# Optimization experiments

Measured on AMD Instinct MI355X. Metric: run time of the kernel, lower is better.

The kernel has to match this reference:

```python
import jax, jax.numpy as jnp
import numpy as np
from jax import lax

AB = np.array([[-37.254833,-82.50967,53.254833,98.50967],[-82.50967,-173.01933,98.50967,189.01933],[-173.01933,-354.03867,189.01933,370.03867],[-56.,-56.,72.,72.],[-120.,-120.,136.,136.],[-248.,-248.,264.,264.],[-82.50967,-37.254833,98.50967,53.254833],[-173.01933,-82.50967,189.01933,98.50967],[-354.03867,-173.01933,370.03867,189.01933]],dtype=np.float32)
STRIDE = 16
PRE = 2000    # pre-NMS proposals
POST = 300    # post-NMS proposals
NMS_T = 0.7

def conv(x, w, stride, pad):
    return lax.conv_general_dilated(x, w, (stride, stride), pad,
                                    dimension_numbers=('NCHW', 'OIHW', 'NCHW'))

def setup_inputs() -> dict:
    k = jax.random.split(jax.random.key(0), 16)
    f32 = jnp.float32
    def W(i, shape, fan):
        return jax.random.normal(k[i], shape, f32) / np.sqrt(fan)
    return {
        'x':    jax.random.normal(k[0], (1, 3, 608, 1008), f32),
        'Wext': W(1, (512, 3, 16, 16), 3 * 16 * 16),        # stand-in stride-16 extractor
        'Wc1':  W(2, (512, 512, 3, 3), 512 * 9), 'bc1': jnp.zeros((512,), f32),
        'Wloc': W(3, (36, 512, 1, 1), 512) * 0.1, 'bloc': jnp.zeros((36,), f32),
        'Wsc':  W(4, (18, 512, 1, 1), 512), 'bsc': jnp.zeros((18,), f32),
        'W1':   W(5, (25088, 4096), 25088), 'b1': jnp.zeros((4096,), f32),
        'W2':   W(6, (4096, 4096), 4096),  'b2': jnp.zeros((4096,), f32),
        'Wl':   W(7, (4096, 84), 4096),    'bl': jnp.zeros((84,), f32),
        'Ws':   W(8, (4096, 21), 4096),    'bs': jnp.zeros((21,), f32),
        'scale': 2,
    }

def _anchors(h, w):
    yy = jnp.arange(h, dtype=jnp.float32) * STRIDE
    xx = jnp.arange(w, dtype=jnp.float32) * STRIDE
    sy, sx = jnp.meshgrid(yy, xx, indexing='ij')
    shift = jnp.stack([sy.ravel(), sx.ravel(), sy.ravel(), sx.ravel()], axis=1)  # [h*w,4]
    return (jnp.asarray(AB)[None, :, :] + shift[:, None, :]).reshape(-1, 4)      # [h*w*9,4]

def _loc2bbox(a, loc):
    ph = a[:, 2] - a[:, 0]; pw = a[:, 3] - a[:, 1]
    py = a[:, 0] + 0.5 * ph; px = a[:, 1] + 0.5 * pw
    cy = loc[:, 0] * ph + py; cx = loc[:, 1] * pw + px
    hh = jnp.exp(loc[:, 2]) * ph; ww = jnp.exp(loc[:, 3]) * pw
    return jnp.stack([cy - 0.5 * hh, cx - 0.5 * ww, cy + 0.5 * hh, cx + 0.5 * ww], axis=1)

def _nms(boxes, valid):
    # greedy sequential NMS, boxes pre-sorted by score desc; +1 area convention as in source
    n = boxes.shape[0]
    areas = (boxes[:, 2] - boxes[:, 0] + 1.) * (boxes[:, 3] - boxes[:, 1] + 1.)
    idx = jnp.arange(n)
    def body(i, keep):
        b = boxes[i]
        iy1 = jnp.maximum(b[0], boxes[:, 0]); ix1 = jnp.maximum(b[1], boxes[:, 1])
        iy2 = jnp.minimum(b[2], boxes[:, 2]); ix2 = jnp.minimum(b[3], boxes[:, 3])
        inter = jnp.clip(iy2 - iy1 + 1., 0) * jnp.clip(ix2 - ix1 + 1., 0)
        iou = inter / (areas[i] + areas - inter)
        sup = (iou > NMS_T) & (idx > i)
        return jnp.where(keep[i], keep & ~sup, keep)  # suppressed boxes don't suppress
    return lax.fori_loop(0, n, body, valid)

def _roi_maxpool(feat, rois):
    # feat [C,h,w]; adaptive max pool each integer ROI crop to 7x7 (matches AdaptiveMaxPool2d bins)
    C, h, w = feat.shape
    yy = jnp.arange(h); xx = jnp.arange(w); i7 = jnp.arange(7)
    NEG = jnp.float32(-1e30)
    def one(box):
        t = jnp.floor(box / STRIDE).astype(jnp.int32)
        y0 = jnp.clip(t[0], 0, h - 1); x0 = jnp.clip(t[1], 0, w - 1)
        y1 = jnp.clip(t[2], 0, h - 1); x1 = jnp.clip(t[3], 0, w - 1)
        H = y1 - y0 + 1; W_ = x1 - x0 + 1
        rs = y0 + (i7 * H) // 7;  re = y0 + ((i7 + 1) * H + 6) // 7
        cs = x0 + (i7 * W_) // 7; ce = x0 + ((i7 + 1) * W_ + 6) // 7
        rowm = (yy[None, :] >= rs[:, None]) & (yy[None, :] < re[:, None])  # [7,h]
        colm = (xx[None, :] >= cs[:, None]) & (xx[None, :] < ce[:, None])  # [7,w]
        tmp = jnp.max(jnp.where(colm[None, None, :, :], feat[:, :, None, :], NEG), axis=-1)  # [C,h,7]
        return jnp.max(jnp.where(rowm[None, :, :, None], tmp[:, None, :, :], NEG), axis=2)   # [C,7,7]
    return lax.map(one, rois)

def reference(x, Wext, Wc1, bc1, Wloc, bloc, Wsc, bsc, W1, b1, W2, b2, Wl, bl, Ws, bs, scale):
    Himg, Wimg = x.shape[2], x.shape[3]
    feat = jax.nn.relu(conv(x, Wext, STRIDE, 'VALID'))                 # [1,512,h,w]
    h, w = feat.shape[2], feat.shape[3]
    layer1 = jax.nn.relu(conv(feat, Wc1, 1, 'SAME') + bc1[None, :, None, None])
    rpn_locs = (conv(layer1, Wloc, 1, 'SAME') + bloc[None, :, None, None]).transpose(0, 2, 3, 1).reshape(-1, 4)
    sc = (conv(layer1, Wsc, 1, 'SAME') + bsc[None, :, None, None]).transpose(0, 2, 3, 1).reshape(h, w, 9, 2)
    fg = sc[..., 1].reshape(-1)
    anchor = _anchors(h, w)
    roi = _loc2bbox(anchor, rpn_locs)
    roi = jnp.stack([jnp.clip(roi[:, 0], 0, Himg), jnp.clip(roi[:, 1], 0, Wimg),
                     jnp.clip(roi[:, 2], 0, Himg), jnp.clip(roi[:, 3], 0, Wimg)], axis=1)
    min_size = 16. * scale
    valid = ((roi[:, 2] - roi[:, 0]) >= min_size) & ((roi[:, 3] - roi[:, 1]) >= min_size)
    s = jnp.where(valid, fg, -jnp.inf)      # masked instead of filtered (jit-friendly)
    order = jnp.argsort(-s)[:PRE]
    boxes = roi[order]; vb = valid[order]
    keep = _nms(boxes, vb)
    sel = jnp.argsort(jnp.where(keep, 0, PRE) + jnp.arange(PRE))[:POST]  # kept boxes first, index order
    rois = lax.stop_gradient(boxes[sel])                                 # [300,4], detached as in source
    pool = _roi_maxpool(feat[0], rois).reshape(POST, -1)                 # [300,25088]
    fc7 = jax.nn.relu(jax.nn.relu(pool @ W1 + b1) @ W2 + b2)
    return (fc7 @ Wl + bl, fc7 @ Ws + bs, rois)
```

## Files before the change

### kernel.cpp

```cpp
#include <hip/hip_runtime.h>
#include <stdint.h>

#define FH 38
#define FW 63
#define NPOS 2394
#define NANCH 21546
#define HIMG 608
#define WIMG 1008
#define PRE 2000
#define POST 300

typedef __attribute__((ext_vector_type(8))) short bf16x8;
typedef __attribute__((ext_vector_type(4))) float f32x4;

__device__ __constant__ float c_AB[9][4] = {
  {-37.254833f,-82.50967f,53.254833f,98.50967f},
  {-82.50967f,-173.01933f,98.50967f,189.01933f},
  {-173.01933f,-354.03867f,189.01933f,370.03867f},
  {-56.f,-56.f,72.f,72.f},
  {-120.f,-120.f,136.f,136.f},
  {-248.f,-248.f,264.f,264.f},
  {-82.50967f,-37.254833f,98.50967f,53.254833f},
  {-173.01933f,-82.50967f,189.01933f,98.50967f},
  {-354.03867f,-173.01933f,370.03867f,189.01933f}};

__device__ __forceinline__ unsigned short f2bf(float f) {
  unsigned u = __float_as_uint(f);
  u += 0x7FFFu + ((u >> 16) & 1u);
  return (unsigned short)(u >> 16);
}

__global__ __launch_bounds__(256) void k_wc1pack(const float* __restrict__ Wc1, float* __restrict__ Bp) {
  __shared__ float t[4608];
  int o = blockIdx.x;
  const float* src = Wc1 + (size_t)o * 4608;
  for (int i = threadIdx.x; i < 4608; i += 256) t[i] = src[i];
  __syncthreads();
  float* dst = Bp + (size_t)o * 4608;
  for (int i = threadIdx.x; i < 4608; i += 256) {
    int r = i >> 9, ci = i & 511;
    dst[i] = t[ci * 9 + r];
  }
}

template<int MODE>
__global__ __launch_bounds__(256) void k_gemm_conv(
    const float* __restrict__ src, const float* __restrict__ B,
    float* __restrict__ P, int Kc)
{
  const int K = MODE ? 4608 : 768;
  __shared__ float As[16][132];
  __shared__ float Bs[16][68];
  int tid = threadIdx.x;
  int bm = blockIdx.x * 128, bn = blockIdx.y * 64;
  int k0 = blockIdx.z * Kc;
  int kend = k0 + Kc;
  int tx = tid & 15, ty = tid >> 4;
  float4 acc[8];
  #pragma unroll
  for (int i = 0; i < 8; ++i) acc[i] = make_float4(0.f, 0.f, 0.f, 0.f);
  int lr = tid >> 2, lk = (tid & 3) * 4;
  int ar0 = bm + lr;      if (ar0 >= NPOS) ar0 = NPOS - 1;
  int ar1 = bm + lr + 64; if (ar1 >= NPOS) ar1 = NPOS - 1;
  int py0 = ar0 / FW, px0 = ar0 - py0 * FW;
  int py1 = ar1 / FW, px1 = ar1 - py1 * FW;
  const float* bp = B + (size_t)(bn + lr) * K + lk;

  float4 ra0, ra1, rb;
  auto loadA = [&](int kk, float4& v0, float4& v1) {
    if (MODE == 0) {
      int ci = kk >> 8, ky = (kk >> 4) & 15;
      const float* base = src + (size_t)(ci * HIMG + ky) * WIMG + lk;
      v0 = *(const float4*)(base + (size_t)(py0 * 16) * WIMG + px0 * 16);
      v1 = *(const float4*)(base + (size_t)(py1 * 16) * WIMG + px1 * 16);
    } else {
      int r = kk >> 9, cb = (kk & 511) + lk;
      int q = r / 3;
      int dy = q - 1, dx = r - q * 3 - 1;
      int yy0 = py0 + dy, xx0 = px0 + dx;
      int yy1 = py1 + dy, xx1 = px1 + dx;
      v0 = ((unsigned)yy0 < FH && (unsigned)xx0 < FW)
           ? *(const float4*)(src + (((size_t)(yy0 * FW + xx0)) << 9) + cb)
           : make_float4(0.f, 0.f, 0.f, 0.f);
      v1 = ((unsigned)yy1 < FH && (unsigned)xx1 < FW)
           ? *(const float4*)(src + (((size_t)(yy1 * FW + xx1)) << 9) + cb)
           : make_float4(0.f, 0.f, 0.f, 0.f);
    }
  };
  loadA(k0, ra0, ra1);
  rb = *(const float4*)(bp + k0);

  for (; k0 < kend; k0 += 16) {
    As[lk + 0][lr] = ra0.x; As[lk + 1][lr] = ra0.y; As[lk + 2][lr] = ra0.z; As[lk + 3][lr] = ra0.w;
    As[lk + 0][lr + 64] = ra1.x; As[lk + 1][lr + 64] = ra1.y; As[lk + 2][lr + 64] = ra1.z; As[lk + 3][lr + 64] = ra1.w;
    Bs[lk + 0][lr] = rb.x; Bs[lk + 1][lr] = rb.y; Bs[lk + 2][lr] = rb.z; Bs[lk + 3][lr] = rb.w;
    __syncthreads();
    if (k0 + 16 < kend) {
      loadA(k0 + 16, ra0, ra1);
      rb = *(const float4*)(bp + k0 + 16);
    }
    #pragma unroll
    for (int k = 0; k < 16; ++k) {
      float4 aL = *(const float4*)&As[k][ty * 8];
      float4 aH = *(const float4*)&As[k][ty * 8 + 4];
      float4 b  = *(const float4*)&Bs[k][tx * 4];
      float av0 = aL.x, av1 = aL.y, av2 = aL.z, av3 = aL.w;
      float av4 = aH.x, av5 = aH.y, av6 = aH.z, av7 = aH.w;
      acc[0].x += av0 * b.x; acc[0].y += av0 * b.y; acc[0].z += av0 * b.z; acc[0].w += av0 * b.w;
      acc[1].x += av1 * b.x; acc[1].y += av1 * b.y; acc[1].z += av1 * b.z; acc[1].w += av1 * b.w;
      acc[2].x += av2 * b.x; acc[2].y += av2 * b.y; acc[2].z += av2 * b.z; acc[2].w += av2 * b.w;
      acc[3].x += av3 * b.x; acc[3].y += av3 * b.y; acc[3].z += av3 * b.z; acc[3].w += av3 * b.w;
      acc[4].x += av4 * b.x; acc[4].y += av4 * b.y; acc[4].z += av4 * b.z; acc[4].w += av4 * b.w;
      acc[5].x += av5 * b.x; acc[5].y += av5 * b.y; acc[5].z += av5 * b.z; acc[5].w += av5 * b.w;
      acc[6].x += av6 * b.x; acc[6].y += av6 * b.y; acc[6].z += av6 * b.z; acc[6].w += av6 * b.w;
      acc[7].x += av7 * b.x; acc[7].y += av7 * b.y; acc[7].z += av7 * b.z; acc[7].w += av7 * b.w;
    }
    __syncthreads();
  }
  float* Pp = P + (size_t)blockIdx.z * NPOS * 512;
  #pragma unroll
  for (int i = 0; i < 8; ++i) {
    int m = bm + ty * 8 + i;
    if (m < NPOS) *(float4*)&Pp[(size_t)m * 512 + bn + tx * 4] = acc[i];
  }
}

template<bool BIAS, int S>
__global__ __launch_bounds__(256) void k_reduce_conv(
    const float* __restrict__ P, const float* __restrict__ bias,
    float* __restrict__ C)
{
  int i = blockIdx.x * 256 + threadIdx.x;
  if (i >= NPOS * 128) return;
  size_t stride = (size_t)NPOS * 512;
  float4 s = make_float4(0.f, 0.f, 0.f, 0.f);
  if (BIAS) s = *(const float4*)&bias[(i * 4) & 511];
  #pragma unroll
  for (int s2 = 0; s2 < S; ++s2) {
    float4 v = *(const float4*)&P[s2 * stride + (size_t)i * 4];
    s.x += v.x; s.y += v.y; s.z += v.z; s.w += v.w;
  }
  s.x = fmaxf(s.x, 0.f); s.y = fmaxf(s.y, 0.f); s.z = fmaxf(s.z, 0.f); s.w = fmaxf(s.w, 0.f);
  *(float4*)&C[(size_t)i * 4] = s;
}

__global__ __launch_bounds__(256) void k_gemm_rpn(
    const float* __restrict__ A, const float* __restrict__ Wloc, const float* __restrict__ Wsc,
    const float* __restrict__ bloc, const float* __restrict__ bsc,
    float* __restrict__ rpnloc, float* __restrict__ rpnsc)
{
  __shared__ float As[16][68];
  __shared__ float Bs[16][68];
  int tid = threadIdx.x;
  int bm = blockIdx.x * 64;
  int tx = tid & 15, ty = tid >> 4;
  float acc[4][4] = {};
  int lr = tid >> 2, lk = (tid & 3) * 4;
  int ar = bm + lr; if (ar >= NPOS) ar = NPOS - 1;
  const float* ap = A + (size_t)ar * 512 + lk;
  const float* bp;
  if (lr < 36)      bp = Wloc + (size_t)lr * 512 + lk;
  else if (lr < 54) bp = Wsc + (size_t)(lr - 36) * 512 + lk;
  else              bp = Wsc + lk;
  for (int k0 = 0; k0 < 512; k0 += 16) {
    float4 av = *(const float4*)(ap + k0);
    float4 bv = *(const float4*)(bp + k0);
    As[lk + 0][lr] = av.x; As[lk + 1][lr] = av.y; As[lk + 2][lr] = av.z; As[lk + 3][lr] = av.w;
    Bs[lk + 0][lr] = bv.x; Bs[lk + 1][lr] = bv.y; Bs[lk + 2][lr] = bv.z; Bs[lk + 3][lr] = bv.w;
    __syncthreads();
    #pragma unroll
    for (int k = 0; k < 16; ++k) {
      float4 a = *(const float4*)&As[k][ty * 4];
      float4 b = *(const float4*)&Bs[k][tx * 4];
      acc[0][0] += a.x * b.x; acc[0][1] += a.x * b.y; acc[0][2] += a.x * b.z; acc[0][3] += a.x * b.w;
      acc[1][0] += a.y * b.x; acc[1][1] += a.y * b.y; acc[1][2] += a.y * b.z; acc[1][3] += a.y * b.w;
      acc[2][0] += a.z * b.x; acc[2][1] += a.z * b.y; acc[2][2] += a.z * b.z; acc[2][3] += a.z * b.w;
      acc[3][0] += a.w * b.x; acc[3][1] += a.w * b.y; acc[3][2] += a.w * b.z; acc[3][3] += a.w * b.w;
    }
    __syncthreads();
  }
  #pragma unroll
  for (int i = 0; i < 4; ++i) {
    int m = bm + ty * 4 + i;
    if (m >= NPOS) continue;
    #pragma unroll
    for (int j = 0; j < 4; ++j) {
      int n = tx * 4 + j;
      if (n < 36)      rpnloc[(size_t)m * 36 + n] = acc[i][j] + bloc[n];
      else if (n < 54) rpnsc[(size_t)m * 18 + (n - 36)] = acc[i][j] + bsc[n - 36];
    }
  }
}

__global__ __launch_bounds__(256) void k_proposal(
    const float* __restrict__ rpnloc, const float* __restrict__ rpnsc,
    const void* __restrict__ scalep, float4* __restrict__ roi_all,
    unsigned long long* __restrict__ keys)
{
  int a = blockIdx.x * 256 + threadIdx.x;
  if (a >= NANCH) return;
  int s = a / 9, t = a - s * 9;
  int iy = s / FW, ix = s - iy * FW;
  float sy = iy * 16.f, sx = ix * 16.f;
  float ay1 = c_AB[t][0] + sy, ax1 = c_AB[t][1] + sx;
  float ay2 = c_AB[t][2] + sy, ax2 = c_AB[t][3] + sx;
  const float* lp = rpnloc + (size_t)s * 36 + t * 4;
  float dy = lp[0], dx = lp[1], dh = lp[2], dw = lp[3];
  float ph = ay2 - ay1, pw = ax2 - ax1;
  float py = ay1 + 0.5f * ph, px = ax1 + 0.5f * pw;
  float cy = dy * ph + py, cx = dx * pw + px;
  float hh = expf(dh) * ph, ww = expf(dw) * pw;
  float y1 = cy - 0.5f * hh, x1 = cx - 0.5f * ww;
  float y2 = cy + 0.5f * hh, x2 = cx + 0.5f * ww;
  y1 = fminf(fmaxf(y1, 0.f), (float)HIMG); y2 = fminf(fmaxf(y2, 0.f), (float)HIMG);
  x1 = fminf(fmaxf(x1, 0.f), (float)WIMG); x2 = fminf(fmaxf(x2, 0.f), (float)WIMG);
  int iv = *(const int*)scalep;
  float scale = (iv >= 1 && iv < 1000000) ? (float)iv : *(const float*)scalep;
  float minsz = 16.f * scale;
  bool valid = (y2 - y1 >= minsz) && (x2 - x1 >= minsz);
  float fg = rpnsc[(size_t)s * 18 + t * 2 + 1];
  float sc = valid ? fg : __uint_as_float(0xFF800000u);
  unsigned u = __float_as_uint(sc);
  u = (u & 0x80000000u) ? ~u : (u | 0x80000000u);
  keys[a] = (((unsigned long long)(~u)) << 32) | (unsigned)a;
  roi_all[a] = make_float4(y1, x1, y2, x2);
}

__global__ __launch_bounds__(1024) void k_topk(
    const unsigned long long* __restrict__ keys, const float4* __restrict__ roi_all,
    float4* __restrict__ boxes, int* __restrict__ vbs)
{
  __shared__ unsigned int hist[256];
  __shared__ unsigned long long prefix;
  __shared__ int rankr;
  __shared__ int cnt;
  __shared__ unsigned long long sk[2048];
  int tid = threadIdx.x;
  if (tid == 0) { prefix = 0ULL; rankr = PRE - 1; }
  __syncthreads();
  for (int p = 7; p >= 0; --p) {
    if (tid < 256) hist[tid] = 0;
    __syncthreads();
    unsigned long long pref = prefix;
    int shift = (p + 1) * 8;
    for (int i = tid; i < NANCH; i += 1024) {
      unsigned long long k = keys[i];
      bool match = (p == 7) || ((k >> shift) == (pref >> shift));
      if (match) atomicAdd(&hist[(unsigned)(k >> (p * 8)) & 255u], 1u);
    }
    __syncthreads();
    if (tid == 0) {
      int r = rankr;
      unsigned cum = 0;
      for (int b2 = 0; b2 < 256; ++b2) {
        unsigned c = hist[b2];
        if (cum + c > (unsigned)r) { prefix |= ((unsigned long long)b2) << (p * 8); rankr = r - (int)cum; break; }
        cum += c;
      }
    }
    __syncthreads();
  }
  unsigned long long kth = prefix;
  if (tid == 0) cnt = 0;
  __syncthreads();
  for (int i = tid; i < NANCH; i += 1024) {
    unsigned long long k = keys[i];
    if (k <= kth) {
      int pos = atomicAdd(&cnt, 1);
      if (pos < 2048) sk[pos] = k;
    }
  }
  __syncthreads();
  if (tid < 48) sk[2000 + tid] = ~0ULL;
  __syncthreads();
  for (int size = 2; size <= 2048; size <<= 1) {
    for (int stride = size >> 1; stride > 0; stride >>= 1) {
      int i = 2 * tid - (tid & (stride - 1));
      int j = i + stride;
      unsigned long long a = sk[i], b = sk[j];
      bool asc = ((i & size) == 0);
      bool sw = asc ? (a > b) : (a < b);
      __syncthreads();
      if (sw) { sk[i] = b; sk[j] = a; }
      __syncthreads();
    }
  }
  for (int i = tid; i < PRE; i += 1024) {
    unsigned long long k = sk[i];
    int a = (int)(k & 0xFFFFFFFFULL);
    boxes[i] = roi_all[a];
    vbs[i] = ((unsigned)(k >> 32) < 0xFF800000u) ? 1 : 0;
  }
}

__global__ __launch_bounds__(64) void k_supmat(const float4* __restrict__ boxes,
                                               unsigned long long* __restrict__ supmat)
{
  int i = blockIdx.x;
  int lane = threadIdx.x;
  float4 bi = boxes[i];
  float ai = (bi.z - bi.x + 1.f) * (bi.w - bi.y + 1.f);
  for (int w = 0; w < 32; ++w) {
    int j = w * 64 + lane;
    bool sup = false;
    if (j < PRE && j > i) {
      float4 bj = boxes[j];
      float aj = (bj.z - bj.x + 1.f) * (bj.w - bj.y + 1.f);
      float iy1 = fmaxf(bi.x, bj.x), ix1 = fmaxf(bi.y, bj.y);
      float iy2 = fminf(bi.z, bj.z), ix2 = fminf(bi.w, bj.w);
      float ih = fmaxf(iy2 - iy1 + 1.f, 0.f), iw = fmaxf(ix2 - ix1 + 1.f, 0.f);
      float inter = ih * iw;
      float iou = inter / (ai + aj - inter);
      sup = iou > 0.7f;
    }
    unsigned long long word = __ballot(sup);
    if (lane == 0) supmat[(size_t)i * 32 + w] = word;
  }
}

__global__ __launch_bounds__(256) void k_nms(
    const unsigned long long* __restrict__ supmat, const int* __restrict__ vbs,
    const float4* __restrict__ boxes, float* __restrict__ rois_ws, float* __restrict__ out_rois)
{
  __shared__ unsigned long long rows[64][32];
  __shared__ unsigned long long removed[32];
  __shared__ unsigned long long keepw[32];
  __shared__ unsigned long long kmsh;
  __shared__ int pref[33];
  __shared__ int sel[2048];
  int tid = threadIdx.x;
  if (tid < 32) removed[tid] = 0ULL;
  __syncthreads();
  for (int b = 0; b < 32; ++b) {
    for (int t = tid; t < 2048; t += 256) {
      int k = t >> 5, w = t & 31;
      rows[k][w] = supmat[(size_t)(b * 64 + k) * 32 + w];
    }
    __syncthreads();
    if (tid < 64) {
      int lane = tid;
      int gj = b * 64 + lane;
      int vb = (gj < PRE) ? vbs[gj] : 0;
      unsigned long long vbw = __ballot(vb != 0);
      unsigned long long km = vbw & ~removed[b];
      unsigned long long Wj = rows[lane][b];
      for (int k = 0; k < 64; ++k) {
        unsigned long long wk = __shfl(Wj, k);
        if ((km >> k) & 1ULL) km &= ~wk;
      }
      if (lane == 0) { keepw[b] = km; kmsh = km; }
    }
    __syncthreads();
    {
      unsigned long long km = kmsh;
      int w = tid & 31, kb = (tid >> 5) * 8;
      unsigned long long acc = 0ULL;
      for (int k = kb; k < kb + 8; ++k)
        if ((km >> k) & 1ULL) acc |= rows[k][w];
      if (acc) atomicOr((unsigned long long*)&removed[w], acc);
    }
    __syncthreads();
  }
  if (tid == 0) {
    pref[0] = 0;
    for (int w = 0; w < 32; ++w) pref[w + 1] = pref[w] + __popcll(keepw[w]);
  }
  __syncthreads();
  if (tid < 32) {
    int w = tid;
    unsigned long long bits = keepw[w];
    int base = pref[w], r = 0;
    for (int bit = 0; bit < 64; ++bit)
      if ((bits >> bit) & 1ULL) { sel[base + r] = w * 64 + bit; r++; }
    int Kc = pref[32];
    unsigned long long mask = (w < 31) ? ~0ULL : 0xFFFFULL;
    unsigned long long ub = ~keepw[w] & mask;
    int ubase = Kc + (w * 64 - pref[w]); r = 0;
    for (int bit = 0; bit < 64; ++bit)
      if ((ub >> bit) & 1ULL) { sel[ubase + r] = w * 64 + bit; r++; }
  }
  __syncthreads();
  for (int t = tid; t < POST; t += 256) {
    float4 bx = boxes[sel[t]];
    rois_ws[t * 4 + 0] = bx.x; rois_ws[t * 4 + 1] = bx.y;
    rois_ws[t * 4 + 2] = bx.z; rois_ws[t * 4 + 3] = bx.w;
    out_rois[t * 4 + 0] = bx.x; out_rois[t * 4 + 1] = bx.y;
    out_rois[t * 4 + 2] = bx.z; out_rois[t * 4 + 3] = bx.w;
  }
}

__global__ __launch_bounds__(256) void k_roipool(
    const float* __restrict__ feat_yxc, const float* __restrict__ rois,
    unsigned short* __restrict__ poolbf)
{
  int r = blockIdx.x, cg = blockIdx.y;
  int lane = threadIdx.x & 63, bslot = threadIdx.x >> 6;
  int c = cg * 64 + lane;
  float b0 = rois[r * 4 + 0], b1 = rois[r * 4 + 1], b2 = rois[r * 4 + 2], b3 = rois[r * 4 + 3];
  int y0 = min(max((int)floorf(b0 * 0.0625f), 0), FH - 1);
  int x0 = min(max((int)floorf(b1 * 0.0625f), 0), FW - 1);
  int y1 = min(max((int)floorf(b2 * 0.0625f), 0), FH - 1);
  int x1 = min(max((int)floorf(b3 * 0.0625f), 0), FW - 1);
  int Hh = y1 - y0 + 1, Ww = x1 - x0 + 1;
  for (int bin = bslot; bin < 49; bin += 4) {
    int by = bin / 7, bx = bin - by * 7;
    int rs = y0 + (by * Hh) / 7, re = y0 + ((by + 1) * Hh + 6) / 7;
    int cs = x0 + (bx * Ww) / 7, ce = x0 + ((bx + 1) * Ww + 6) / 7;
    float m = -1e30f;
    for (int y = rs; y < re; ++y)
      for (int x = cs; x < ce; ++x)
        m = fmaxf(m, feat_yxc[((size_t)(y * FW + x)) * 512 + c]);
    poolbf[(size_t)r * 25088 + c * 49 + bin] = f2bf(m);
  }
}

template<bool BBF16>
__global__ __launch_bounds__(512) void k_fcg(
    const unsigned short* __restrict__ A, const void* __restrict__ Bv,
    float* __restrict__ P, int K, int N)
{
  __shared__ unsigned short As[160 * 40];
  __shared__ unsigned short Bs[128 * 40];
  int tid = threadIdx.x;
  int bn = blockIdx.x * 128;
  int bm = blockIdx.y * 160;
  int sk2 = blockIdx.z;
  int KC = K >> 3;
  int k0beg = sk2 * KC, kend = k0beg + KC;
  int w = tid >> 6, lane = tid & 63;
  int wm = w >> 2, wn = w & 3;
  int l15 = lane & 15, lg = lane >> 4;
  int arow0 = tid >> 2, aq0 = tid & 3;
  int arow1 = 128 + (tid >> 2);
  int kr = tid >> 4, bm_ = tid & 15, nn = bm_ * 8;
  int bpos = (((kr >> 3) ^ (bm_ & 3)) << 3) | (kr & 7);
  const float* Bf = (const float*)Bv;
  const unsigned short* Bh = (const unsigned short*)Bv;

  f32x4 acc[5][2];
  #pragma unroll
  for (int a_ = 0; a_ < 5; ++a_) {
    acc[a_][0] = (f32x4){0.f, 0.f, 0.f, 0.f};
    acc[a_][1] = (f32x4){0.f, 0.f, 0.f, 0.f};
  }

  uint4 ra0, ra1, rbh;
  float4 rb0, rb1;
  ra0 = *(const uint4*)(A + (size_t)(bm + arow0) * K + k0beg + aq0 * 8);
  if (tid < 128) ra1 = *(const uint4*)(A + (size_t)(bm + arow1) * K + k0beg + aq0 * 8);
  if (BBF16) rbh = *(const uint4*)(Bh + (size_t)(k0beg + kr) * N + bn + nn);
  else {
    rb0 = *(const float4*)(Bf + (size_t)(k0beg + kr) * N + bn + nn);
    rb1 = *(const float4*)(Bf + (size_t)(k0beg + kr) * N + bn + nn + 4);
  }

  for (int k0 = k0beg; k0 < kend; k0 += 32) {
    *(uint4*)(&As[arow0 * 40 + aq0 * 8]) = ra0;
    if (tid < 128) *(uint4*)(&As[arow1 * 40 + aq0 * 8]) = ra1;
    {
      unsigned short bb[8];
      if (BBF16) {
        const unsigned short* pp = (const unsigned short*)&rbh;
        #pragma unroll
        for (int j = 0; j < 8; ++j) bb[j] = pp[j];
      } else {
        bb[0] = f2bf(rb0.x); bb[1] = f2bf(rb0.y); bb[2] = f2bf(rb0.z); bb[3] = f2bf(rb0.w);
        bb[4] = f2bf(rb1.x); bb[5] = f2bf(rb1.y); bb[6] = f2bf(rb1.z); bb[7] = f2bf(rb1.w);
      }
      #pragma unroll
      for (int j = 0; j < 8; ++j) Bs[(nn + j) * 40 + bpos] = bb[j];
    }
    __syncthreads();
    if (k0 + 32 < kend) {
      ra0 = *(const uint4*)(A + (size_t)(bm + arow0) * K + k0 + 32 + aq0 * 8);
      if (tid < 128) ra1 = *(const uint4*)(A + (size_t)(bm + arow1) * K + k0 + 32 + aq0 * 8);
      if (BBF16) rbh = *(const uint4*)(Bh + (size_t)(k0 + 32 + kr) * N + bn + nn);
      else {
        rb0 = *(const float4*)(Bf + (size_t)(k0 + 32 + kr) * N + bn + nn);
        rb1 = *(const float4*)(Bf + (size_t)(k0 + 32 + kr) * N + bn + nn + 4);
      }
    }
    bf16x8 bf[2];
    #pragma unroll
    for (int ns = 0; ns < 2; ++ns) {
      int n = wn * 32 + ns * 16 + l15;
      int g = lg ^ ((n >> 3) & 3);
      bf[ns] = *(const bf16x8*)(&Bs[n * 40 + g * 8]);
    }
    #pragma unroll
    for (int mt = 0; mt < 5; ++mt) {
      int row = wm * 80 + mt * 16 + l15;
      bf16x8 af = *(const bf16x8*)(&As[row * 40 + lg * 8]);
      acc[mt][0] = __builtin_amdgcn_mfma_f32_16x16x32_bf16(af, bf[0], acc[mt][0], 0, 0, 0);
      acc[mt][1] = __builtin_amdgcn_mfma_f32_16x16x32_bf16(af, bf[1], acc[mt][1], 0, 0, 0);
    }
    __syncthreads();
  }
  float* Pp = P + (size_t)sk2 * 320 * N;
  #pragma unroll
  for (int mt = 0; mt < 5; ++mt)
    #pragma unroll
    for (int ns = 0; ns < 2; ++ns)
      #pragma unroll
      for (int r2 = 0; r2 < 4; ++r2) {
        int m = bm + wm * 80 + mt * 16 + lg * 4 + r2;
        int n = bn + wn * 32 + ns * 16 + l15;
        Pp[(size_t)m * N + n] = acc[mt][ns][r2];
      }
}

__global__ __launch_bounds__(256) void k_wpack(
    const float* __restrict__ Wl, const float* __restrict__ Wsv, unsigned short* __restrict__ Wcat)
{
  int idx = blockIdx.x * 256 + threadIdx.x;
  if (idx >= 4096 * 128) return;
  int k = idx >> 7, n = idx & 127;
  float v = 0.f;
  if (n < 84) v = Wl[(size_t)k * 84 + n];
  else if (n < 105) v = Wsv[(size_t)k * 21 + (n - 84)];
  Wcat[idx] = f2bf(v);
}

__global__ __launch_bounds__(256) void k_headreduce(
    const float* __restrict__ P, const float* __restrict__ bl, const float* __restrict__ bs,
    float* __restrict__ out)
{
  int idx = blockIdx.x * 256 + threadIdx.x;
  if (idx >= 300 * 105) return;
  int m = idx / 105, n = idx - m * 105;
  float s = 0.f;
  #pragma unroll
  for (int s2 = 0; s2 < 8; ++s2) s += P[(size_t)s2 * 320 * 128 + m * 128 + n];
  if (n < 84) out[(size_t)m * 84 + n] = s + bl[n];
  else        out[25200 + (size_t)m * 21 + (n - 84)] = s + bs[n - 84];
}

__global__ __launch_bounds__(256) void k_reduce1(
    const float* __restrict__ P, const float* __restrict__ b1, unsigned short* __restrict__ h1bf)
{
  int idx = blockIdx.x * 256 + threadIdx.x;
  if (idx >= 320 * 4096) return;
  int m = idx >> 12, n = idx & 4095;
  float s = b1[n];
  #pragma unroll
  for (int s2 = 0; s2 < 8; ++s2) s += P[(size_t)s2 * 320 * 4096 + idx];
  s = fmaxf(s, 0.f);
  h1bf[idx] = (m < 300) ? f2bf(s) : (unsigned short)0;
}

__global__ __launch_bounds__(256) void k_reduce2(
    const float* __restrict__ P, const float* __restrict__ b2, unsigned short* __restrict__ fc7bf)
{
  int idx = blockIdx.x * 256 + threadIdx.x;
  if (idx >= 300 * 4096) return;
  int n = idx & 4095;
  float s = b2[n];
  #pragma unroll
  for (int s2 = 0; s2 < 8; ++s2) s += P[(size_t)s2 * 320 * 4096 + idx];
  fc7bf[idx] = f2bf(fmaxf(s, 0.f));
}

extern "C" void kernel_launch(void* const* d_in, const int* in_sizes, int n_in,
                              void* d_out, int out_size, void* d_ws, size_t ws_size,
                              hipStream_t stream)
{
  const float* x    = (const float*)d_in[0];
  const float* Wext = (const float*)d_in[1];
  const float* Wc1  = (const float*)d_in[2];
  const float* bc1  = (const float*)d_in[3];
  const float* Wloc = (const float*)d_in[4];
  const float* bloc = (const float*)d_in[5];
  const float* Wsc  = (const float*)d_in[6];
  const float* bsc  = (const float*)d_in[7];
  const float* W1   = (const float*)d_in[8];
  const float* b1   = (const float*)d_in[9];
  const float* W2   = (const float*)d_in[10];
  const float* b2   = (const float*)d_in[11];
  const float* Wl   = (const float*)d_in[12];
  const float* bl   = (const float*)d_in[13];
  const float* Wsv  = (const float*)d_in[14];
  const float* bs   = (const float*)d_in[15];
  const void*  scalep = d_in[16];
  float* out = (float*)d_out;
  char* ws = (char*)d_ws;

  size_t off = 0;
  auto alloc = [&](size_t b) { size_t o = off; off += (b + 255) & ~(size_t)255; return o; };
  size_t o_featyxc = alloc((size_t)NPOS * 512 * 4);
  size_t o_layer1  = alloc((size_t)NPOS * 512 * 4);
  size_t o_rpnloc  = alloc((size_t)NPOS * 36 * 4);
  size_t o_rpnsc   = alloc((size_t)NPOS * 18 * 4);
  size_t o_roiall  = alloc((size_t)NANCH * 16);
  size_t o_keys    = alloc((size_t)NANCH * 8);
  size_t o_boxes   = alloc((size_t)PRE * 16);
  size_t o_vbs     = alloc((size_t)PRE * 4);
  size_t o_supmat  = alloc((size_t)PRE * 32 * 8);
  size_t o_rois    = alloc((size_t)POST * 16);
  size_t o_poolbf  = alloc((size_t)320 * 25088 * 2);
  size_t o_h1bf    = alloc((size_t)320 * 4096 * 2);
  size_t o_wcat    = alloc((size_t)4096 * 128 * 2);
  size_t o_wc1p    = alloc((size_t)512 * 4608 * 4);
  size_t o_cpart   = alloc((size_t)8 * NPOS * 512 * 4);
  size_t o_part    = alloc((size_t)8 * 320 * 4096 * 4);
  (void)ws_size; (void)in_sizes; (void)n_in; (void)out_size;

  float* feat_yxc = (float*)(ws + o_featyxc);
  float* layer1   = (float*)(ws + o_layer1);
  float* rpnloc   = (float*)(ws + o_rpnloc);
  float* rpnsc    = (float*)(ws + o_rpnsc);
  float4* roi_all = (float4*)(ws + o_roiall);
  unsigned long long* keys = (unsigned long long*)(ws + o_keys);
  float4* boxes   = (float4*)(ws + o_boxes);
  int* vbs        = (int*)(ws + o_vbs);
  unsigned long long* supmat = (unsigned long long*)(ws + o_supmat);
  float* rois     = (float*)(ws + o_rois);
  unsigned short* poolbf = (unsigned short*)(ws + o_poolbf);
  unsigned short* h1bf   = (unsigned short*)(ws + o_h1bf);
  unsigned short* wcat   = (unsigned short*)(ws + o_wcat);
  float* wc1p     = (float*)(ws + o_wc1p);
  float* cpart    = (float*)(ws + o_cpart);
  float* partials = (float*)(ws + o_part);

  k_wpack<<<(4096 * 128) / 256, 256, 0, stream>>>(Wl, Wsv, wcat);
  k_wc1pack<<<512, 256, 0, stream>>>(Wc1, wc1p);
  k_gemm_conv<0><<<dim3(19, 8, 4), 256, 0, stream>>>(x, Wext, cpart, 192);
  k_reduce_conv<false, 4><<<(NPOS * 128 + 255) / 256, 256, 0, stream>>>(cpart, nullptr, feat_yxc);
  k_gemm_conv<1><<<dim3(19, 8, 8), 256, 0, stream>>>(feat_yxc, wc1p, cpart, 576);
  k_reduce_conv<true, 8><<<(NPOS * 128 + 255) / 256, 256, 0, stream>>>(cpart, bc1, layer1);
  k_gemm_rpn<<<38, 256, 0, stream>>>(layer1, Wloc, Wsc, bloc, bsc, rpnloc, rpnsc);
  k_proposal<<<(NANCH + 255) / 256, 256, 0, stream>>>(rpnloc, rpnsc, scalep, roi_all, keys);
  k_topk<<<1, 1024, 0, stream>>>(keys, roi_all, boxes, vbs);
  k_supmat<<<PRE, 64, 0, stream>>>(boxes, supmat);
  k_nms<<<1, 256, 0, stream>>>(supmat, vbs, boxes, rois, out + 31500);
  k_roipool<<<dim3(POST, 8), 256, 0, stream>>>(feat_yxc, rois, poolbf);
  k_fcg<false><<<dim3(32, 2, 8), 512, 0, stream>>>(poolbf, W1, partials, 25088, 4096);
  k_reduce1<<<(320 * 4096) / 256, 256, 0, stream>>>(partials, b1, h1bf);
  k_fcg<false><<<dim3(32, 2, 8), 512, 0, stream>>>(h1bf, W2, partials, 4096, 4096);
  k_reduce2<<<(300 * 4096) / 256, 256, 0, stream>>>(partials, b2, h1bf);
  k_fcg<true><<<dim3(1, 2, 8), 512, 0, stream>>>(h1bf, wcat, partials, 4096, 128);
  k_headreduce<<<(300 * 105 + 255) / 256, 256, 0, stream>>>(partials, bl, bs, out);
}
```

Before: 769.9 us.

## Split single-block top-k into select, parallel compact, and rank-sort kernels

The single-block top-k kernel is split into three kernels. Radix select stays in one block, but compaction now runs across many blocks with a global atomic counter. The bitonic sort over 2048 keys is replaced by a multi-block rank sort, where each thread counts how many candidates are smaller to find its output slot. This removes the long chain of block-wide barriers in the bitonic network, at the cost of two extra launches and O(n^2) comparisons, which the LDS absorbs.

Result: no change. 777.3 us (+1.0%).

```diff
diff --git a/kernel.cpp b/kernel.cpp
--- a/kernel.cpp
+++ b/kernel.cpp
@@ -226,15 +226,12 @@
   roi_all[a] = make_float4(y1, x1, y2, x2);
 }
 
-__global__ __launch_bounds__(1024) void k_topk(
-    const unsigned long long* __restrict__ keys, const float4* __restrict__ roi_all,
-    float4* __restrict__ boxes, int* __restrict__ vbs)
+__global__ __launch_bounds__(1024) void k_select(
+    const unsigned long long* __restrict__ keys, unsigned long long* __restrict__ kthbuf)
 {
   __shared__ unsigned int hist[256];
   __shared__ unsigned long long prefix;
   __shared__ int rankr;
-  __shared__ int cnt;
-  __shared__ unsigned long long sk[2048];
   int tid = threadIdx.x;
   if (tid == 0) { prefix = 0ULL; rankr = PRE - 1; }
   __syncthreads();
@@ -260,37 +257,39 @@
     }
     __syncthreads();
   }
-  unsigned long long kth = prefix;
-  if (tid == 0) cnt = 0;
+  if (tid == 0) { kthbuf[0] = prefix; kthbuf[1] = 0ULL; }
+}
+
+__global__ __launch_bounds__(256) void k_compact(
+    const unsigned long long* __restrict__ keys, unsigned long long* __restrict__ kthbuf,
+    unsigned long long* __restrict__ cand)
+{
+  int i = blockIdx.x * 256 + threadIdx.x;
+  if (i >= NANCH) return;
+  unsigned long long kth = kthbuf[0];
+  unsigned long long k = keys[i];
+  if (k <= kth) {
+    unsigned pos = atomicAdd((unsigned*)&kthbuf[1], 1u);
+    if (pos < PRE) cand[pos] = k;
+  }
+}
+
+__global__ __launch_bounds__(256) void k_rank(
+    const unsigned long long* __restrict__ cand, const float4* __restrict__ roi_all,
+    float4* __restrict__ boxes, int* __restrict__ vbs)
+{
+  __shared__ unsigned long long sk[PRE];
+  int tid = threadIdx.x;
+  for (int i = tid; i < PRE; i += 256) sk[i] = cand[i];
   __syncthreads();
-  for (int i = tid; i < NANCH; i += 1024) {
-    unsigned long long k = keys[i];
-    if (k <= kth) {
-      int pos = atomicAdd(&cnt, 1);
-      if (pos < 2048) sk[pos] = k;
-    }
-  }
-  __syncthreads();
-  if (tid < 48) sk[2000 + tid] = ~0ULL;
-  __syncthreads();
-  for (int size = 2; size <= 2048; size <<= 1) {
-    for (int stride = size >> 1; stride > 0; stride >>= 1) {
-      int i = 2 * tid - (tid & (stride - 1));
-      int j = i + stride;
-      unsigned long long a = sk[i], b = sk[j];
-      bool asc = ((i & size) == 0);
-      bool sw = asc ? (a > b) : (a < b);
-      __syncthreads();
-      if (sw) { sk[i] = b; sk[j] = a; }
-      __syncthreads();
-    }
-  }
-  for (int i = tid; i < PRE; i += 1024) {
-    unsigned long long k = sk[i];
-    int a = (int)(k & 0xFFFFFFFFULL);
-    boxes[i] = roi_all[a];
-    vbs[i] = ((unsigned)(k >> 32) < 0xFF800000u) ? 1 : 0;
-  }
+  int i = blockIdx.x * 256 + tid;
+  if (i >= PRE) return;
+  unsigned long long my = sk[i];
+  int rank = 0;
+  for (int j = 0; j < PRE; ++j) rank += (sk[j] < my) ? 1 : 0;
+  int a = (int)(my & 0xFFFFFFFFULL);
+  boxes[rank] = roi_all[a];
+  vbs[rank] = ((unsigned)(my >> 32) < 0xFF800000u) ? 1 : 0;
 }
 
 __global__ __launch_bounds__(64) void k_supmat(const float4* __restrict__ boxes,
@@ -592,6 +591,8 @@
   size_t o_rpnsc   = alloc((size_t)NPOS * 18 * 4);
   size_t o_roiall  = alloc((size_t)NANCH * 16);
   size_t o_keys    = alloc((size_t)NANCH * 8);
+  size_t o_kth     = alloc((size_t)256);
+  size_t o_cand    = alloc((size_t)PRE * 8);
   size_t o_boxes   = alloc((size_t)PRE * 16);
   size_t o_vbs     = alloc((size_t)PRE * 4);
   size_t o_supmat  = alloc((size_t)PRE * 32 * 8);
@@ -610,6 +611,8 @@
   float* rpnsc    = (float*)(ws + o_rpnsc);
   float4* roi_all = (float4*)(ws + o_roiall);
   unsigned long long* keys = (unsigned long long*)(ws + o_keys);
+  unsigned long long* kthbuf = (unsigned long long*)(ws + o_kth);
+  unsigned long long* cand = (unsigned long long*)(ws + o_cand);
   float4* boxes   = (float4*)(ws + o_boxes);
   int* vbs        = (int*)(ws + o_vbs);
   unsigned long long* supmat = (unsigned long long*)(ws + o_supmat);
@@ -629,7 +632,9 @@
   k_reduce_conv<true, 8><<<(NPOS * 128 + 255) / 256, 256, 0, stream>>>(cpart, bc1, layer1);
   k_gemm_rpn<<<38, 256, 0, stream>>>(layer1, Wloc, Wsc, bloc, bsc, rpnloc, rpnsc);
   k_proposal<<<(NANCH + 255) / 256, 256, 0, stream>>>(rpnloc, rpnsc, scalep, roi_all, keys);
-  k_topk<<<1, 1024, 0, stream>>>(keys, roi_all, boxes, vbs);
+  k_select<<<1, 1024, 0, stream>>>(keys, kthbuf);
+  k_compact<<<(NANCH + 255) / 256, 256, 0, stream>>>(keys, kthbuf, cand);
+  k_rank<<<(PRE + 255) / 256, 256, 0, stream>>>(cand, roi_all, boxes, vbs);
   k_supmat<<<PRE, 64, 0, stream>>>(boxes, supmat);
   k_nms<<<1, 256, 0, stream>>>(supmat, vbs, boxes, rois, out + 31500);
   k_roipool<<<dim3(POST, 8), 256, 0, stream>>>(feat_yxc, rois, poolbf);
```
